# Kernel tuning notes

Hardware: AMD Instinct MI355X
Metric: run time of the kernel (lower is better)

## Reference

```python
import jax, jax.numpy as jnp
import numpy as np

IN_FEATURES = 4096
OUT_FEATURES = 4096
NNZ = 838860
BATCH = 512


def setup_inputs() -> dict:
    key = jax.random.key(0)
    kx, kr, kc, kv, kb = jax.random.split(key, 5)
    x = jax.random.normal(kx, (BATCH, IN_FEATURES), dtype=jnp.float32)
    row_idx = jax.random.randint(kr, (NNZ,), 0, OUT_FEATURES, dtype=jnp.int64)
    col_idx = jax.random.randint(kc, (NNZ,), 0, IN_FEATURES, dtype=jnp.int64)
    values = jax.random.normal(kv, (NNZ,), dtype=jnp.float32)
    bias = jax.random.normal(kb, (OUT_FEATURES,), dtype=jnp.float32)
    return {"x": x, "row_idx": row_idx, "col_idx": col_idx,
            "values": values, "bias": bias}


def reference(x, row_idx, col_idx, values, bias):
    # COO sparse linear: y[b, row] += x[b, col] * val, then add bias.
    x_flat = x.reshape(-1, IN_FEATURES)                    # [B, in]
    weighted = x_flat[:, col_idx] * values                 # [B, nnz]
    out = jnp.zeros((x_flat.shape[0], OUT_FEATURES), dtype=x.dtype)
    out = out.at[:, row_idx].add(weighted)                 # scatter-add per row
    out = out + bias
    return out.reshape(x.shape[:-1] + (OUT_FEATURES,))
```

## Files before the change

kernel.cpp:

```cpp
#include <hip/hip_runtime.h>

#define IN_F   4096
#define OUT_F  4096
#define K_DIM  4096
#define NNZ_C  838860
#define BATCH  512
#define SPLITK 2
#define KS     (K_DIM / SPLITK)
#define BK     32
#define BM     64
#define BN     128

typedef short bf16x8 __attribute__((ext_vector_type(8)));
typedef float f32x4  __attribute__((ext_vector_type(4)));

__device__ __forceinline__ unsigned short f2bf(float f) {
    unsigned u = __float_as_uint(f);
    u += 0x7fffu + ((u >> 16) & 1u);
    return (unsigned short)(u >> 16);
}
__device__ __forceinline__ float bf2f(unsigned short h) {
    return __uint_as_float((unsigned)h << 16);
}
__device__ __forceinline__ void gload_lds16(const void* g, void* l) {
    __builtin_amdgcn_global_load_lds(
        (const __attribute__((address_space(1))) unsigned int*)g,
        (__attribute__((address_space(3))) unsigned int*)l, 16, 0, 0);
}

__global__ void convert_x(const float* __restrict__ x,
                          unsigned short* __restrict__ xb) {
    int i = blockIdx.x * 256 + threadIdx.x;
    const float4* p = (const float4*)x + (size_t)i * 2;
    float4 a = p[0], b = p[1];
    union { unsigned short h[8]; bf16x8 v; } u;
    u.h[0] = f2bf(a.x); u.h[1] = f2bf(a.y); u.h[2] = f2bf(a.z); u.h[3] = f2bf(a.w);
    u.h[4] = f2bf(b.x); u.h[5] = f2bf(b.y); u.h[6] = f2bf(b.z); u.h[7] = f2bf(b.w);
    ((bf16x8*)xb)[i] = u.v;
}

__global__ void scatter_w(const int* __restrict__ row_idx,
                          const int* __restrict__ col_idx,
                          const float* __restrict__ values,
                          unsigned* __restrict__ W) {
    int i = blockIdx.x * 256 + threadIdx.x;
    if (i >= NNZ_C) return;
    size_t idx = (size_t)row_idx[i] * (size_t)K_DIM + (size_t)col_idx[i];
    float v = values[i];
    unsigned* wp = &W[idx >> 1];
    int hi = (int)(idx & 1);
    unsigned old = *wp, assumed;
    do {
        assumed = old;
        unsigned short cur = hi ? (unsigned short)(assumed >> 16)
                                : (unsigned short)(assumed & 0xffffu);
        unsigned short nh = f2bf(bf2f(cur) + v);
        unsigned nw = hi ? ((assumed & 0x0000ffffu) | ((unsigned)nh << 16))
                         : ((assumed & 0xffff0000u) | (unsigned)nh);
        old = atomicCAS(wp, assumed, nw);
    } while (old != assumed);
}

template <int EPI>
__global__ void __launch_bounds__(256)
gemm_bt(const unsigned short* __restrict__ Abf,
        const unsigned short* __restrict__ Wbf,
        const float* __restrict__ bias,
        float* __restrict__ out,
        float* __restrict__ part) {
    __shared__ __align__(16) unsigned short As[BM * BK];
    __shared__ __align__(16) unsigned short Bs[BN * BK];

    const int nt = blockIdx.x, mt = blockIdx.y, s = blockIdx.z;
    const int t = threadIdx.x, w = t >> 6, ln = t & 63;
    const int ks0 = s * KS;

    const int arow = mt * BM + w * 16 + (ln >> 2);
    const int brow = nt * BN + w * 16 + (ln >> 2);
    const unsigned short* gA  = Abf + (size_t)arow * K_DIM + ks0 + (ln & 3) * 8;
    const unsigned short* gB0 = Wbf + (size_t)brow * K_DIM + ks0 + (ln & 3) * 8;
    const unsigned short* gB1 = gB0 + (size_t)64 * K_DIM;
    unsigned short* lA  = &As[(w * 16) * BK];
    unsigned short* lB0 = &Bs[(w * 16) * BK];
    unsigned short* lB1 = &Bs[(64 + w * 16) * BK];

    const int quad = ln >> 4, lanem = ln & 15;
    const unsigned short* rA = &As[lanem * BK + quad * 8];
    const unsigned short* rB = &Bs[(w * 32 + lanem) * BK + quad * 8];

    float bv0 = bias[nt * BN + w * 32 + lanem];
    float bv1 = bias[nt * BN + w * 32 + 16 + lanem];
    f32x4 acc[4][2];
    for (int mi = 0; mi < 4; ++mi) {
        float i0 = (s == 0) ? bv0 : 0.f;
        float i1 = (s == 0) ? bv1 : 0.f;
        acc[mi][0] = (f32x4){i0, i0, i0, i0};
        acc[mi][1] = (f32x4){i1, i1, i1, i1};
    }

    for (int kt = 0; kt < KS / BK; ++kt) {
        __syncthreads();
        gload_lds16(gA  + kt * BK, lA);
        gload_lds16(gB0 + kt * BK, lB0);
        gload_lds16(gB1 + kt * BK, lB1);
        __syncthreads();

        bf16x8 af0 = *(const bf16x8*)(rA);
        bf16x8 af1 = *(const bf16x8*)(rA + 16 * BK);
        bf16x8 af2 = *(const bf16x8*)(rA + 32 * BK);
        bf16x8 af3 = *(const bf16x8*)(rA + 48 * BK);
        bf16x8 bf0 = *(const bf16x8*)(rB);
        bf16x8 bf1 = *(const bf16x8*)(rB + 16 * BK);

        acc[0][0] = __builtin_amdgcn_mfma_f32_16x16x32_bf16(af0, bf0, acc[0][0], 0, 0, 0);
        acc[1][0] = __builtin_amdgcn_mfma_f32_16x16x32_bf16(af1, bf0, acc[1][0], 0, 0, 0);
        acc[2][0] = __builtin_amdgcn_mfma_f32_16x16x32_bf16(af2, bf0, acc[2][0], 0, 0, 0);
        acc[3][0] = __builtin_amdgcn_mfma_f32_16x16x32_bf16(af3, bf0, acc[3][0], 0, 0, 0);
        acc[0][1] = __builtin_amdgcn_mfma_f32_16x16x32_bf16(af0, bf1, acc[0][1], 0, 0, 0);
        acc[1][1] = __builtin_amdgcn_mfma_f32_16x16x32_bf16(af1, bf1, acc[1][1], 0, 0, 0);
        acc[2][1] = __builtin_amdgcn_mfma_f32_16x16x32_bf16(af2, bf1, acc[2][1], 0, 0, 0);
        acc[3][1] = __builtin_amdgcn_mfma_f32_16x16x32_bf16(af3, bf1, acc[3][1], 0, 0, 0);
    }

    const int col0 = nt * BN + w * 32 + lanem;
    const int row0 = mt * BM + quad * 4;
    for (int mi = 0; mi < 4; ++mi) {
        for (int ni = 0; ni < 2; ++ni) {
            int c = col0 + ni * 16;
            for (int r = 0; r < 4; ++r) {
                size_t o = (size_t)(row0 + mi * 16 + r) * OUT_F + c;
                if (EPI == 0) {
                    float* dst = (s == 0) ? out : part;
                    dst[o] = acc[mi][ni][r];
                } else {
                    atomicAdd(&out[o], acc[mi][ni][r]);
                }
            }
        }
    }
}

__global__ void reduce_part(float* __restrict__ out, const float* __restrict__ part) {
    int i = blockIdx.x * 256 + threadIdx.x;
    float4 a = ((const float4*)out)[i];
    float4 b = ((const float4*)part)[i];
    a.x += b.x; a.y += b.y; a.z += b.z; a.w += b.w;
    ((float4*)out)[i] = a;
}

extern "C" void kernel_launch(void* const* d_in, const int* in_sizes, int n_in,
                              void* d_out, int out_size, void* d_ws, size_t ws_size,
                              hipStream_t stream) {
    const float* x       = (const float*)d_in[0];
    const int*   row_idx = (const int*)d_in[1];
    const int*   col_idx = (const int*)d_in[2];
    const float* values  = (const float*)d_in[3];
    const float* bias    = (const float*)d_in[4];
    float*       out     = (float*)d_out;

    size_t off = 0;
    unsigned short* xb = (unsigned short*)((char*)d_ws + off);
    off += (size_t)BATCH * K_DIM * 2;
    unsigned* W = (unsigned*)((char*)d_ws + off);
    off += (size_t)OUT_F * K_DIM * 2;
    float* part = (float*)((char*)d_ws + off);
    off += (size_t)BATCH * OUT_F * 4;
    bool use_part = (ws_size >= off);

    hipMemsetAsync(W, 0, (size_t)OUT_F * K_DIM * 2, stream);
    convert_x<<<1024, 256, 0, stream>>>(x, xb);
    scatter_w<<<(NNZ_C + 255) / 256, 256, 0, stream>>>(row_idx, col_idx, values, W);

    if (use_part) {
        gemm_bt<0><<<dim3(32, 8, SPLITK), 256, 0, stream>>>(
            xb, (const unsigned short*)W, bias, out, part);
        reduce_part<<<2048, 256, 0, stream>>>(out, part);
    } else {
        hipMemsetAsync(out, 0, (size_t)BATCH * OUT_F * 4, stream);
        gemm_bt<1><<<dim3(32, 8, SPLITK), 256, 0, stream>>>(
            xb, (const unsigned short*)W, bias, out, nullptr);
    }
}
```

Baseline: 167.5 us.

## Enlarge GEMM tiles, raise split-K, and replace CAS scatter with bitmap dedup

The weight scatter now marks each destination in a bitmap with atomicOr and writes the bf16 value with a plain store. Only duplicate indices go to an overflow list, which a second kernel merges with the old CAS loop. The GEMM block tile grows to 128x128, with each wave computing a 64x64 sub-tile of 4x4 MFMAs for more operand reuse per LDS load. Split-K rises to 4 with three partial buffers reduced at the end, which adds partial-sum memory traffic, an extra bitmap memset and a fixed overflow capacity.

```diff
diff --git a/kernel.cpp b/kernel.cpp
--- a/kernel.cpp
+++ b/kernel.cpp
@@ -1,15 +1,16 @@
 #include <hip/hip_runtime.h>
 
-#define IN_F   4096
-#define OUT_F  4096
-#define K_DIM  4096
-#define NNZ_C  838860
-#define BATCH  512
-#define SPLITK 2
-#define KS     (K_DIM / SPLITK)
-#define BK     32
-#define BM     64
-#define BN     128
+#define IN_F    4096
+#define OUT_F   4096
+#define K_DIM   4096
+#define NNZ_C   838860
+#define BATCH   512
+#define SPLITK  4
+#define KS      (K_DIM / SPLITK)
+#define BK      32
+#define BM      128
+#define BN      128
+#define OVF_CAP 131072
 
 typedef short bf16x8 __attribute__((ext_vector_type(8)));
 typedef float f32x4  __attribute__((ext_vector_type(4)));
@@ -39,15 +40,36 @@
     ((bf16x8*)xb)[i] = u.v;
 }
 
-__global__ void scatter_w(const int* __restrict__ row_idx,
-                          const int* __restrict__ col_idx,
-                          const float* __restrict__ values,
-                          unsigned* __restrict__ W) {
+__global__ void scatter_mark(const int* __restrict__ row_idx,
+                             const int* __restrict__ col_idx,
+                             const float* __restrict__ values,
+                             unsigned short* __restrict__ W,
+                             unsigned* __restrict__ bitmap,
+                             uint2* __restrict__ ovf,
+                             int* __restrict__ ovf_cnt) {
     int i = blockIdx.x * 256 + threadIdx.x;
     if (i >= NNZ_C) return;
-    size_t idx = (size_t)row_idx[i] * (size_t)K_DIM + (size_t)col_idx[i];
-    float v = values[i];
-    unsigned* wp = &W[idx >> 1];
+    unsigned idx = (unsigned)row_idx[i] * K_DIM + (unsigned)col_idx[i];
+    unsigned bit = 1u << (idx & 31);
+    unsigned old = atomicOr(&bitmap[idx >> 5], bit);
+    if (old & bit) {
+        int p = atomicAdd(ovf_cnt, 1);
+        if (p < OVF_CAP) ovf[p] = make_uint2(idx, __float_as_uint(values[i]));
+    } else {
+        W[idx] = f2bf(values[i]);
+    }
+}
+
+__global__ void fix_dups(const uint2* __restrict__ ovf,
+                         const int* __restrict__ ovf_cnt,
+                         unsigned* __restrict__ W32) {
+    int i = blockIdx.x * 256 + threadIdx.x;
+    int n = min(*ovf_cnt, OVF_CAP);
+    if (i >= n) return;
+    uint2 e = ovf[i];
+    unsigned idx = e.x;
+    float v = __uint_as_float(e.y);
+    unsigned* wp = &W32[idx >> 1];
     int hi = (int)(idx & 1);
     unsigned old = *wp, assumed;
     do {
@@ -61,90 +83,126 @@
     } while (old != assumed);
 }
 
+__global__ void scatter_cas(const int* __restrict__ row_idx,
+                            const int* __restrict__ col_idx,
+                            const float* __restrict__ values,
+                            unsigned* __restrict__ W32) {
+    int i = blockIdx.x * 256 + threadIdx.x;
+    if (i >= NNZ_C) return;
+    size_t idx = (size_t)row_idx[i] * K_DIM + (size_t)col_idx[i];
+    float v = values[i];
+    unsigned* wp = &W32[idx >> 1];
+    int hi = (int)(idx & 1);
+    unsigned old = *wp, assumed;
+    do {
+        assumed = old;
+        unsigned short cur = hi ? (unsigned short)(assumed >> 16)
+                                : (unsigned short)(assumed & 0xffffu);
+        unsigned short nh = f2bf(bf2f(cur) + v);
+        unsigned nw = hi ? ((assumed & 0x0000ffffu) | ((unsigned)nh << 16))
+                         : ((assumed & 0xffff0000u) | (unsigned)nh);
+        old = atomicCAS(wp, assumed, nw);
+    } while (old != assumed);
+}
+
 template <int EPI>
 __global__ void __launch_bounds__(256)
 gemm_bt(const unsigned short* __restrict__ Abf,
         const unsigned short* __restrict__ Wbf,
         const float* __restrict__ bias,
         float* __restrict__ out,
-        float* __restrict__ part) {
+        float* __restrict__ parts) {
     __shared__ __align__(16) unsigned short As[BM * BK];
     __shared__ __align__(16) unsigned short Bs[BN * BK];
 
     const int nt = blockIdx.x, mt = blockIdx.y, s = blockIdx.z;
     const int t = threadIdx.x, w = t >> 6, ln = t & 63;
+    const int wm = w & 1, wn = w >> 1;
     const int ks0 = s * KS;
 
-    const int arow = mt * BM + w * 16 + (ln >> 2);
-    const int brow = nt * BN + w * 16 + (ln >> 2);
-    const unsigned short* gA  = Abf + (size_t)arow * K_DIM + ks0 + (ln & 3) * 8;
-    const unsigned short* gB0 = Wbf + (size_t)brow * K_DIM + ks0 + (ln & 3) * 8;
+    const int srow = w * 16 + (ln >> 2);
+    const int scol = (ln & 3) * 8;
+    const unsigned short* gA0 = Abf + (size_t)(mt * BM + srow) * K_DIM + ks0 + scol;
+    const unsigned short* gA1 = gA0 + (size_t)64 * K_DIM;
+    const unsigned short* gB0 = Wbf + (size_t)(nt * BN + srow) * K_DIM + ks0 + scol;
     const unsigned short* gB1 = gB0 + (size_t)64 * K_DIM;
-    unsigned short* lA  = &As[(w * 16) * BK];
+    unsigned short* lA0 = &As[(w * 16) * BK];
+    unsigned short* lA1 = &As[(64 + w * 16) * BK];
     unsigned short* lB0 = &Bs[(w * 16) * BK];
     unsigned short* lB1 = &Bs[(64 + w * 16) * BK];
 
     const int quad = ln >> 4, lanem = ln & 15;
-    const unsigned short* rA = &As[lanem * BK + quad * 8];
-    const unsigned short* rB = &Bs[(w * 32 + lanem) * BK + quad * 8];
-
-    float bv0 = bias[nt * BN + w * 32 + lanem];
-    float bv1 = bias[nt * BN + w * 32 + 16 + lanem];
-    f32x4 acc[4][2];
-    for (int mi = 0; mi < 4; ++mi) {
-        float i0 = (s == 0) ? bv0 : 0.f;
-        float i1 = (s == 0) ? bv1 : 0.f;
-        acc[mi][0] = (f32x4){i0, i0, i0, i0};
-        acc[mi][1] = (f32x4){i1, i1, i1, i1};
-    }
+    const unsigned short* rA = &As[(wm * 64 + lanem) * BK + quad * 8];
+    const unsigned short* rB = &Bs[(wn * 64 + lanem) * BK + quad * 8];
+
+    float bv[4];
+#pragma unroll
+    for (int ni = 0; ni < 4; ++ni)
+        bv[ni] = bias[nt * BN + wn * 64 + ni * 16 + lanem];
+
+    f32x4 acc[4][4];
+#pragma unroll
+    for (int mi = 0; mi < 4; ++mi)
+#pragma unroll
+        for (int ni = 0; ni < 4; ++ni) {
+            float iv = (s == 0) ? bv[ni] : 0.f;
+            acc[mi][ni] = (f32x4){iv, iv, iv, iv};
+        }
 
     for (int kt = 0; kt < KS / BK; ++kt) {
         __syncthreads();
-        gload_lds16(gA  + kt * BK, lA);
+        gload_lds16(gA0 + kt * BK, lA0);
+        gload_lds16(gA1 + kt * BK, lA1);
         gload_lds16(gB0 + kt * BK, lB0);
         gload_lds16(gB1 + kt * BK, lB1);
         __syncthreads();
 
-        bf16x8 af0 = *(const bf16x8*)(rA);
-        bf16x8 af1 = *(const bf16x8*)(rA + 16 * BK);
-        bf16x8 af2 = *(const bf16x8*)(rA + 32 * BK);
-        bf16x8 af3 = *(const bf16x8*)(rA + 48 * BK);
-        bf16x8 bf0 = *(const bf16x8*)(rB);
-        bf16x8 bf1 = *(const bf16x8*)(rB + 16 * BK);
-
-        acc[0][0] = __builtin_amdgcn_mfma_f32_16x16x32_bf16(af0, bf0, acc[0][0], 0, 0, 0);
-        acc[1][0] = __builtin_amdgcn_mfma_f32_16x16x32_bf16(af1, bf0, acc[1][0], 0, 0, 0);
-        acc[2][0] = __builtin_amdgcn_mfma_f32_16x16x32_bf16(af2, bf0, acc[2][0], 0, 0, 0);
-        acc[3][0] = __builtin_amdgcn_mfma_f32_16x16x32_bf16(af3, bf0, acc[3][0], 0, 0, 0);
-        acc[0][1] = __builtin_amdgcn_mfma_f32_16x16x32_bf16(af0, bf1, acc[0][1], 0, 0, 0);
-        acc[1][1] = __builtin_amdgcn_mfma_f32_16x16x32_bf16(af1, bf1, acc[1][1], 0, 0, 0);
-        acc[2][1] = __builtin_amdgcn_mfma_f32_16x16x32_bf16(af2, bf1, acc[2][1], 0, 0, 0);
-        acc[3][1] = __builtin_amdgcn_mfma_f32_16x16x32_bf16(af3, bf1, acc[3][1], 0, 0, 0);
-    }
-
-    const int col0 = nt * BN + w * 32 + lanem;
-    const int row0 = mt * BM + quad * 4;
-    for (int mi = 0; mi < 4; ++mi) {
-        for (int ni = 0; ni < 2; ++ni) {
+        bf16x8 af[4], bfr[4];
+#pragma unroll
+        for (int mi = 0; mi < 4; ++mi) af[mi]  = *(const bf16x8*)(rA + mi * 16 * BK);
+#pragma unroll
+        for (int ni = 0; ni < 4; ++ni) bfr[ni] = *(const bf16x8*)(rB + ni * 16 * BK);
+#pragma unroll
+        for (int mi = 0; mi < 4; ++mi)
+#pragma unroll
+            for (int ni = 0; ni < 4; ++ni)
+                acc[mi][ni] = __builtin_amdgcn_mfma_f32_16x16x32_bf16(
+                    af[mi], bfr[ni], acc[mi][ni], 0, 0, 0);
+    }
+
+    const int row0 = mt * BM + wm * 64 + quad * 4;
+    const int col0 = nt * BN + wn * 64 + lanem;
+#pragma unroll
+    for (int mi = 0; mi < 4; ++mi)
+#pragma unroll
+        for (int ni = 0; ni < 4; ++ni) {
             int c = col0 + ni * 16;
+#pragma unroll
             for (int r = 0; r < 4; ++r) {
                 size_t o = (size_t)(row0 + mi * 16 + r) * OUT_F + c;
                 if (EPI == 0) {
-                    float* dst = (s == 0) ? out : part;
+                    float* dst = (s == 0) ? out
+                               : parts + (size_t)(s - 1) * BATCH * OUT_F;
                     dst[o] = acc[mi][ni][r];
                 } else {
                     atomicAdd(&out[o], acc[mi][ni][r]);
                 }
             }
         }
-    }
-}
-
-__global__ void reduce_part(float* __restrict__ out, const float* __restrict__ part) {
-    int i = blockIdx.x * 256 + threadIdx.x;
+}
+
+__global__ void reduce_parts(float* __restrict__ out,
+                             const float* __restrict__ parts) {
+    int i = blockIdx.x * 256 + threadIdx.x;
+    const float4* p0 = (const float4*)parts;
+    const float4* p1 = p0 + (size_t)BATCH * OUT_F / 4;
+    const float4* p2 = p1 + (size_t)BATCH * OUT_F / 4;
     float4 a = ((const float4*)out)[i];
-    float4 b = ((const float4*)part)[i];
-    a.x += b.x; a.y += b.y; a.z += b.z; a.w += b.w;
+    float4 b = p0[i], c = p1[i], d = p2[i];
+    a.x += b.x + c.x + d.x;
+    a.y += b.y + c.y + d.y;
+    a.z += b.z + c.z + d.z;
+    a.w += b.w + c.w + d.w;
     ((float4*)out)[i] = a;
 }
 
@@ -161,23 +219,42 @@
     size_t off = 0;
     unsigned short* xb = (unsigned short*)((char*)d_ws + off);
     off += (size_t)BATCH * K_DIM * 2;
-    unsigned* W = (unsigned*)((char*)d_ws + off);
+    unsigned short* W = (unsigned short*)((char*)d_ws + off);
     off += (size_t)OUT_F * K_DIM * 2;
-    float* part = (float*)((char*)d_ws + off);
-    off += (size_t)BATCH * OUT_F * 4;
-    bool use_part = (ws_size >= off);
+    unsigned* bitmap = (unsigned*)((char*)d_ws + off);
+    off += (size_t)OUT_F * K_DIM / 8;
+    int* ovf_cnt = (int*)((char*)d_ws + off);
+    off += 256;
+    uint2* ovf = (uint2*)((char*)d_ws + off);
+    off += (size_t)OVF_CAP * 8;
+    size_t need_bitmap = off;
+    float* parts = (float*)((char*)d_ws + off);
+    off += (size_t)3 * BATCH * OUT_F * 4;
+    size_t need_parts = off;
+
+    bool use_bitmap = (ws_size >= need_bitmap);
+    bool use_parts  = (ws_size >= need_parts);
 
     hipMemsetAsync(W, 0, (size_t)OUT_F * K_DIM * 2, stream);
     convert_x<<<1024, 256, 0, stream>>>(x, xb);
-    scatter_w<<<(NNZ_C + 255) / 256, 256, 0, stream>>>(row_idx, col_idx, values, W);
-
-    if (use_part) {
-        gemm_bt<0><<<dim3(32, 8, SPLITK), 256, 0, stream>>>(
-            xb, (const unsigned short*)W, bias, out, part);
-        reduce_part<<<2048, 256, 0, stream>>>(out, part);
+
+    if (use_bitmap) {
+        hipMemsetAsync(bitmap, 0, (size_t)OUT_F * K_DIM / 8 + 256, stream);
+        scatter_mark<<<(NNZ_C + 255) / 256, 256, 0, stream>>>(
+            row_idx, col_idx, values, W, bitmap, ovf, ovf_cnt);
+        fix_dups<<<OVF_CAP / 256, 256, 0, stream>>>(ovf, ovf_cnt, (unsigned*)W);
+    } else {
+        scatter_cas<<<(NNZ_C + 255) / 256, 256, 0, stream>>>(
+            row_idx, col_idx, values, (unsigned*)W);
+    }
+
+    if (use_parts) {
+        gemm_bt<0><<<dim3(OUT_F / BN, BATCH / BM, SPLITK), 256, 0, stream>>>(
+            xb, W, bias, out, parts);
+        reduce_parts<<<BATCH * OUT_F / 4 / 256, 256, 0, stream>>>(out, parts);
     } else {
         hipMemsetAsync(out, 0, (size_t)BATCH * OUT_F * 4, stream);
-        gemm_bt<1><<<dim3(32, 8, SPLITK), 256, 0, stream>>>(
-            xb, (const unsigned short*)W, bias, out, nullptr);
-    }
-}
+        gemm_bt<1><<<dim3(OUT_F / BN, BATCH / BM, SPLITK), 256, 0, stream>>>(
+            xb, W, bias, out, nullptr);
+    }
+}
```

New measurement: 246.4 us. 47.1% more time.
